# Optimization experiments

Measured on AMD Instinct MI355X. Metric: run time of the kernel, lower is better.

Reference implementation:

```python
import jax, jax.numpy as jnp
import numpy as np

EPS = 1e-5  # torch LayerNorm default
DT_RANK = 32  # ceil(d_model=512 / 16)


def layer_norm(x, g, b):
    mu = x.mean(-1, keepdims=True)
    var = x.var(-1, keepdims=True)
    return (x - mu) / jnp.sqrt(var + EPS) * g + b


def conv1d(x, w, b, pad):
    # x: (B, C, L), w: (O, I, K) -- torch Conv1d semantics
    y = jax.lax.conv_general_dilated(x, w, (1,), [(pad, pad)],
                                     dimension_numbers=('NCH', 'OIH', 'NCH'))
    return y + b[None, :, None]


def mamba(u, in_w, conv_w, conv_b, xproj_w, dt_w, dt_b, Alog, D, out_w, d_state, d_conv):
    # Faithful mamba_ssm Mamba block (no biases on in/x/out proj, RMS of official impl)
    Bsz, L, _ = u.shape
    xz = jnp.einsum('bld,ed->ble', u, in_w)          # (B, L, 2*Di)
    x, z = jnp.split(xz, 2, axis=-1)
    Di = x.shape[-1]
    # causal depthwise conv1d, truncated to L (padding=d_conv-1 on the left)
    xc = jax.lax.conv_general_dilated(x.transpose(0, 2, 1), conv_w[:, None, :], (1,),
                                      [(d_conv - 1, 0)],
                                      dimension_numbers=('NCH', 'OIH', 'NCH'),
                                      feature_group_count=Di)
    x = jax.nn.silu((xc + conv_b[None, :, None]).transpose(0, 2, 1))  # (B, L, Di)
    xdb = jnp.einsum('bld,ed->ble', x, xproj_w)       # (B, L, dt_rank + 2*N)
    dt = jax.nn.softplus(jnp.einsum('blr,dr->bld', xdb[..., :DT_RANK], dt_w) + dt_b)
    Bm = xdb[..., DT_RANK:DT_RANK + d_state]          # (B, L, N)
    Cm = xdb[..., DT_RANK + d_state:]                 # (B, L, N)
    A = -jnp.exp(Alog)                                # (Di, N)

    def step(h, ins):
        dt_t, x_t, B_t, C_t = ins                     # (B,Di),(B,Di),(B,N),(B,N)
        dA = jnp.exp(dt_t[..., None] * A)             # (B, Di, N)
        h = dA * h + (dt_t * x_t)[..., None] * B_t[:, None, :]
        y = (h * C_t[:, None, :]).sum(-1)             # (B, Di)
        return h, y

    h0 = jnp.zeros((Bsz, Di, d_state), u.dtype)
    xs = (dt.transpose(1, 0, 2), x.transpose(1, 0, 2),
          Bm.transpose(1, 0, 2), Cm.transpose(1, 0, 2))
    _, ys = jax.lax.scan(step, h0, xs)
    y = ys.transpose(1, 0, 2) + x * D                 # skip via D
    y = y * jax.nn.silu(z)
    return jnp.einsum('bld,od->blo', y, out_w)


def _forward(x, fe_w, fe_b, fe_ln_g, fe_ln_b, emb_ln_g, emb_ln_b,
             conv1_w, conv1_b, conv2_w, conv2_b,
             mf_in_w, mf_conv_w, mf_conv_b, mf_xproj_w, mf_dt_w, mf_dt_b, mf_Alog, mf_D, mf_out_w,
             mb_in_w, mb_conv_w, mb_conv_b, mb_xproj_w, mb_dt_w, mb_dt_b, mb_Alog, mb_D, mb_out_w,
             norm_g, norm_b, fc1_w, fc1_b, fc2_w, fc2_b):
    x = x.reshape(x.shape[0], 100, 23)
    # FrequencyEmbedding: rfft over a length-1 last dim == the signal itself; |.| then Linear+LN+ReLU
    id_mag = jnp.abs(x[..., :1])                      # (B, 100, 1)
    e = jax.nn.relu(layer_norm(id_mag @ fe_w.T + fe_b, fe_ln_g, fe_ln_b))
    id_embed = jax.nn.relu(layer_norm(e, emb_ln_g, emb_ln_b))  # outer LN+ReLU
    data = x[..., 1:].transpose(0, 2, 1)              # (B, 22, 100)
    f1 = jax.nn.relu(conv1d(data, conv1_w, conv1_b, 1))
    f2 = jax.nn.relu(conv1d(f1, conv2_w, conv2_b, 1)).transpose(0, 2, 1)  # (B,100,256)
    comb = jnp.concatenate([id_embed, f2], axis=-1)   # (B, 100, 512)
    fo = mamba(comb, mf_in_w, mf_conv_w, mf_conv_b, mf_xproj_w, mf_dt_w, mf_dt_b,
               mf_Alog, mf_D, mf_out_w, 16, 4)
    bo = mamba(comb[:, ::-1], mb_in_w, mb_conv_w, mb_conv_b, mb_xproj_w, mb_dt_w, mb_dt_b,
               mb_Alog, mb_D, mb_out_w, 8, 2)[:, ::-1]
    pooled = (fo + bo).max(axis=1)                    # (B, 512)
    pooled = layer_norm(pooled, norm_g, norm_b)       # self.norm (undefined in source; LN(512))
    h = jax.nn.relu(pooled @ fc1_w.T + fc1_b)
    return h @ fc2_w.T + fc2_b                        # (B, 4)


def setup_inputs() -> dict:
    key = jax.random.key(0)
    ks = iter(jax.random.split(key, 48))
    def n(shape, s=0.02):
        return jax.random.normal(next(ks), shape, jnp.float32) * s
    Di = 1024
    alog16 = jnp.log(jnp.tile(jnp.arange(1, 17, dtype=jnp.float32), (Di, 1)))
    alog8 = jnp.log(jnp.tile(jnp.arange(1, 9, dtype=jnp.float32), (Di, 1)))
    return {
        'x': jax.random.normal(next(ks), (512, 2300), jnp.float32),
        'fe_w': n((256, 1), 1.0), 'fe_b': jnp.zeros(256, jnp.float32),
        'fe_ln_g': jnp.ones(256, jnp.float32), 'fe_ln_b': jnp.zeros(256, jnp.float32),
        'emb_ln_g': jnp.ones(256, jnp.float32), 'emb_ln_b': jnp.zeros(256, jnp.float32),
        'conv1_w': n((128, 22, 3)), 'conv1_b': jnp.zeros(128, jnp.float32),
        'conv2_w': n((256, 128, 3)), 'conv2_b': jnp.zeros(256, jnp.float32),
        'mf_in_w': n((2 * Di, 512)), 'mf_conv_w': n((Di, 4)), 'mf_conv_b': jnp.zeros(Di, jnp.float32),
        'mf_xproj_w': n((32 + 2 * 16, Di)), 'mf_dt_w': n((Di, 32)), 'mf_dt_b': n((Di,), 0.1),
        'mf_Alog': alog16, 'mf_D': jnp.ones(Di, jnp.float32), 'mf_out_w': n((512, Di)),
        'mb_in_w': n((2 * Di, 512)), 'mb_conv_w': n((Di, 2)), 'mb_conv_b': jnp.zeros(Di, jnp.float32),
        'mb_xproj_w': n((32 + 2 * 8, Di)), 'mb_dt_w': n((Di, 32)), 'mb_dt_b': n((Di,), 0.1),
        'mb_Alog': alog8, 'mb_D': jnp.ones(Di, jnp.float32), 'mb_out_w': n((512, Di)),
        'norm_g': jnp.ones(512, jnp.float32), 'norm_b': jnp.zeros(512, jnp.float32),
        'fc1_w': n((128, 512)), 'fc1_b': jnp.zeros(128, jnp.float32),
        'fc2_w': n((4, 128)), 'fc2_b': jnp.zeros(4, jnp.float32),
    }


def reference(x, fe_w, fe_b, fe_ln_g, fe_ln_b, emb_ln_g, emb_ln_b,
              conv1_w, conv1_b, conv2_w, conv2_b,
              mf_in_w, mf_conv_w, mf_conv_b, mf_xproj_w, mf_dt_w, mf_dt_b, mf_Alog, mf_D, mf_out_w,
              mb_in_w, mb_conv_w, mb_conv_b, mb_xproj_w, mb_dt_w, mb_dt_b, mb_Alog, mb_D, mb_out_w,
              norm_g, norm_b, fc1_w, fc1_b, fc2_w, fc2_b):
    return _forward(x, fe_w, fe_b, fe_ln_g, fe_ln_b, emb_ln_g, emb_ln_b,
                    conv1_w, conv1_b, conv2_w, conv2_b,
                    mf_in_w, mf_conv_w, mf_conv_b, mf_xproj_w, mf_dt_w, mf_dt_b, mf_Alog, mf_D, mf_out_w,
                    mb_in_w, mb_conv_w, mb_conv_b, mb_xproj_w, mb_dt_w, mb_dt_b, mb_Alog, mb_D, mb_out_w,
                    norm_g, norm_b, fc1_w, fc1_b, fc2_w, fc2_b)
```

## Files before the change

kernel.cpp:

```cpp
#include <hip/hip_runtime.h>
#include <cstddef>
#include <cstdint>

#define BSZ 512
#define SEQ 100

typedef __bf16 bf16_t;
typedef __attribute__((ext_vector_type(8))) __bf16 bf16x8;
typedef __attribute__((ext_vector_type(4))) float f32x4;

__device__ __forceinline__ float sigmoidf_(float v){ return 1.f/(1.f + __expf(-v)); }
__device__ __forceinline__ float siluf_(float v){ return v * sigmoidf_(v); }
__device__ __forceinline__ float softplusf_(float v){ return (v > 20.f) ? v : __logf(1.f + __expf(v)); }

__global__ __launch_bounds__(256) void cvt_bf16_kernel(
    const float* __restrict__ src, bf16_t* __restrict__ dst, int n)
{
    int i = blockIdx.x*256 + threadIdx.x;
    if (i < n) dst[i] = (bf16_t)src[i];
}

__global__ __launch_bounds__(256) void prep_outw_kernel(
    const float* __restrict__ of, const float* __restrict__ ob, bf16_t* __restrict__ W)
{
    int i = blockIdx.x*256 + threadIdx.x;
    if (i < 512*2048){
        int o = i >> 11, k = i & 2047;
        W[i] = (bf16_t)((k < 1024) ? of[o*1024 + k] : ob[o*1024 + (k - 1024)]);
    }
}

__global__ __launch_bounds__(256) void prep_convw_kernel(
    const float* __restrict__ c1w, const float* __restrict__ c2w,
    bf16_t* __restrict__ W1p, bf16_t* __restrict__ W2p)
{
    int i = blockIdx.x*256 + threadIdx.x;
    if (i < 128*96){
        int o = i / 96, kk = i - o*96, k = kk >> 5, c = kk & 31;
        W1p[i] = (c < 22) ? (bf16_t)c1w[(o*22 + c)*3 + k] : (bf16_t)0.f;
    }
    if (i < 256*384){
        int o = i / 384, kk = i - o*384, k = kk >> 7, c = kk & 127;
        W2p[i] = (bf16_t)c2w[(o*128 + c)*3 + k];
    }
}

__global__ __launch_bounds__(256) void fe0_kernel(
    const float* __restrict__ x,
    const float* __restrict__ fe_w, const float* __restrict__ fe_b,
    const float* __restrict__ g1, const float* __restrict__ b1,
    const float* __restrict__ g2, const float* __restrict__ b2,
    bf16_t* __restrict__ comb, bf16_t* __restrict__ F0pad, bf16_t* __restrict__ F1pad)
{
    const int b = blockIdx.x;
    const int t = threadIdx.x;
    const int wv = t >> 6, lane = t & 63;

    float few[4], feb[4], lg1[4], lb1[4], lg2[4], lb2[4];
    #pragma unroll
    for (int q = 0; q < 4; ++q){
        int j = lane + 64*q;
        few[q] = fe_w[j]; feb[q] = fe_b[j];
        lg1[q] = g1[j];  lb1[q] = b1[j];
        lg2[q] = g2[j];  lb2[q] = b2[j];
    }
    for (int l = wv; l < SEQ; l += 4){
        float m = fabsf(x[(size_t)(b*SEQ + l)*23]);
        float e[4];
        float s1 = 0.f, s2 = 0.f;
        #pragma unroll
        for (int q = 0; q < 4; ++q){ e[q] = m*few[q] + feb[q]; s1 += e[q]; s2 += e[q]*e[q]; }
        #pragma unroll
        for (int off = 32; off > 0; off >>= 1){ s1 += __shfl_xor(s1, off); s2 += __shfl_xor(s2, off); }
        float mean = s1 * (1.f/256.f);
        float rstd = rsqrtf(s2*(1.f/256.f) - mean*mean + 1e-5f);
        s1 = 0.f; s2 = 0.f;
        #pragma unroll
        for (int q = 0; q < 4; ++q){
            e[q] = fmaxf((e[q]-mean)*rstd*lg1[q] + lb1[q], 0.f);
            s1 += e[q]; s2 += e[q]*e[q];
        }
        #pragma unroll
        for (int off = 32; off > 0; off >>= 1){ s1 += __shfl_xor(s1, off); s2 += __shfl_xor(s2, off); }
        mean = s1 * (1.f/256.f);
        rstd = rsqrtf(s2*(1.f/256.f) - mean*mean + 1e-5f);
        #pragma unroll
        for (int q = 0; q < 4; ++q){
            float v = fmaxf((e[q]-mean)*rstd*lg2[q] + lb2[q], 0.f);
            comb[(size_t)(b*SEQ + l)*512 + lane + 64*q] = (bf16_t)v;
        }
    }

    for (int idx = t; idx < 102*32; idx += 256){
        int r = idx >> 5, c = idx & 31;
        float v = 0.f;
        if (r >= 1 && r <= SEQ && c < 22) v = x[(size_t)(b*SEQ + r - 1)*23 + 1 + c];
        F0pad[(size_t)(b*102 + r)*32 + c] = (bf16_t)v;
    }
    if (t < 128) F1pad[(size_t)(b*102 + 0)*128 + t] = (bf16_t)0.f;
    else F1pad[(size_t)(b*102 + 101)*128 + (t - 128)] = (bf16_t)0.f;
}

__global__ __launch_bounds__(256) void gemm_conv_kernel(
    const bf16_t* __restrict__ Abase, int lda, int Az,
    const bf16_t* __restrict__ W, int K, int N,
    const float* __restrict__ bias,
    bf16_t* __restrict__ Cbase, int ldc, int Cb, int coff, int noff, int Mtot)
{
    __shared__ bf16_t As[128*32];
    __shared__ bf16_t Ws[128*32];
    const bf16_t* A = Abase + (size_t)blockIdx.z * Az;
    const int t = threadIdx.x;
    const int lane = t & 63, w = t >> 6;
    const int n0 = blockIdx.y * 128;
    const int rsub = lane >> 2, csub = lane & 3;
    const int col = lane & 15, quad = lane >> 4;
    const int wOffM = (w & 1) * 64, wOffN = (w >> 1) * 64;

    f32x4 acc[4][4];
    #pragma unroll
    for (int i = 0; i < 4; ++i)
        #pragma unroll
        for (int j = 0; j < 4; ++j)
            acc[i][j] = (f32x4){0.f, 0.f, 0.f, 0.f};

    for (int k0 = 0; k0 < K; k0 += 32){
        __syncthreads();
        #pragma unroll
        for (int q = 0; q < 2; ++q){
            const int rt = w*32 + q*16 + rsub;
            const int lq = csub ^ ((rt >> 1) & 3);
            int ra = (rt < Mtot) ? rt : (Mtot - 1);
            const bf16_t* ga = A + (size_t)ra*lda + k0 + lq*8;
            __builtin_amdgcn_global_load_lds(
                (const __attribute__((address_space(1))) void*)ga,
                (__attribute__((address_space(3))) void*)&As[(w*32 + q*16)*32], 16, 0, 0);
            const bf16_t* gw = W + (size_t)(n0 + rt)*K + k0 + lq*8;
            __builtin_amdgcn_global_load_lds(
                (const __attribute__((address_space(1))) void*)gw,
                (__attribute__((address_space(3))) void*)&Ws[(w*32 + q*16)*32], 16, 0, 0);
        }
        __syncthreads();

        bf16x8 af[4], bfv[4];
        #pragma unroll
        for (int i = 0; i < 4; ++i){
            const int ra = wOffM + i*16 + col;
            af[i]  = *(const bf16x8*)&As[ra*32 + (quad ^ ((ra >> 1) & 3))*8];
            const int rb = wOffN + i*16 + col;
            bfv[i] = *(const bf16x8*)&Ws[rb*32 + (quad ^ ((rb >> 1) & 3))*8];
        }
        #pragma unroll
        for (int i = 0; i < 4; ++i)
            #pragma unroll
            for (int j = 0; j < 4; ++j)
                acc[i][j] = __builtin_amdgcn_mfma_f32_16x16x32_bf16(af[i], bfv[j], acc[i][j], 0, 0, 0);
    }

    #pragma unroll
    for (int i = 0; i < 4; ++i){
        const int gmb = wOffM + i*16 + quad*4;
        #pragma unroll
        for (int j = 0; j < 4; ++j){
            const int gn = n0 + wOffN + j*16 + col;
            const float bb = bias[gn];
            #pragma unroll
            for (int r = 0; r < 4; ++r){
                const int gm = gmb + r;
                if (gm < Mtot){
                    float v = fmaxf(acc[i][j][r] + bb, 0.f);
                    Cbase[((size_t)blockIdx.z*Cb + coff + gm)*ldc + noff + gn] = (bf16_t)v;
                }
            }
        }
    }
}

__global__ __launch_bounds__(256) void gemm_in_kernel(
    const bf16_t* __restrict__ A, int lda, int Mtot,
    const bf16_t* __restrict__ W, int K,
    bf16_t* __restrict__ xy, bf16_t* __restrict__ z)
{
    __shared__ bf16_t As[128*32];
    __shared__ bf16_t Ws[128*32];
    const int t = threadIdx.x;
    const int lane = t & 63, w = t >> 6;
    const int m0 = blockIdx.x * 128, n0 = blockIdx.y * 128;
    const int rsub = lane >> 2, csub = lane & 3;
    const int col = lane & 15, quad = lane >> 4;
    const int wOffM = (w & 1) * 64, wOffN = (w >> 1) * 64;

    f32x4 acc[4][4];
    #pragma unroll
    for (int i = 0; i < 4; ++i)
        #pragma unroll
        for (int j = 0; j < 4; ++j)
            acc[i][j] = (f32x4){0.f, 0.f, 0.f, 0.f};

    for (int k0 = 0; k0 < K; k0 += 32){
        __syncthreads();
        #pragma unroll
        for (int q = 0; q < 2; ++q){
            const int rt = w*32 + q*16 + rsub;
            const int lq = csub ^ ((rt >> 1) & 3);
            int ra = m0 + rt; ra = (ra < Mtot) ? ra : (Mtot - 1);
            const bf16_t* ga = A + (size_t)ra*lda + k0 + lq*8;
            __builtin_amdgcn_global_load_lds(
                (const __attribute__((address_space(1))) void*)ga,
                (__attribute__((address_space(3))) void*)&As[(w*32 + q*16)*32], 16, 0, 0);
            const bf16_t* gw = W + (size_t)(n0 + rt)*K + k0 + lq*8;
            __builtin_amdgcn_global_load_lds(
                (const __attribute__((address_space(1))) void*)gw,
                (__attribute__((address_space(3))) void*)&Ws[(w*32 + q*16)*32], 16, 0, 0);
        }
        __syncthreads();

        bf16x8 af[4], bfv[4];
        #pragma unroll
        for (int i = 0; i < 4; ++i){
            const int ra = wOffM + i*16 + col;
            af[i]  = *(const bf16x8*)&As[ra*32 + (quad ^ ((ra >> 1) & 3))*8];
            const int rb = wOffN + i*16 + col;
            bfv[i] = *(const bf16x8*)&Ws[rb*32 + (quad ^ ((rb >> 1) & 3))*8];
        }
        #pragma unroll
        for (int i = 0; i < 4; ++i)
            #pragma unroll
            for (int j = 0; j < 4; ++j)
                acc[i][j] = __builtin_amdgcn_mfma_f32_16x16x32_bf16(af[i], bfv[j], acc[i][j], 0, 0, 0);
    }

    #pragma unroll
    for (int i = 0; i < 4; ++i){
        const int gmb = m0 + wOffM + i*16 + quad*4;
        #pragma unroll
        for (int j = 0; j < 4; ++j){
            const int gn = n0 + wOffN + j*16 + col;
            const int half = gn >> 11, within = gn & 2047;
            const size_t colx = (size_t)(half*1024 + (within & 1023));
            bf16_t* dst = (within < 1024) ? xy : z;
            #pragma unroll
            for (int r = 0; r < 4; ++r){
                const int gm = gmb + r;
                if (gm < Mtot)
                    dst[(size_t)gm*2048 + colx] = (bf16_t)acc[i][j][r];
            }
        }
    }
}

__global__ __launch_bounds__(256) void gemm_out_kernel(
    const bf16_t* __restrict__ A, int Mtot,
    const bf16_t* __restrict__ W,
    float* __restrict__ C)
{
    __shared__ bf16_t As[128*32];
    __shared__ bf16_t Ws[128*32];
    const int t = threadIdx.x;
    const int lane = t & 63, w = t >> 6;
    const int m0 = blockIdx.x * 128, n0 = blockIdx.y * 128;
    const int rsub = lane >> 2, csub = lane & 3;
    const int col = lane & 15, quad = lane >> 4;
    const int wOffM = (w & 1) * 64, wOffN = (w >> 1) * 64;
    const int K = 2048;

    f32x4 acc[4][4];
    #pragma unroll
    for (int i = 0; i < 4; ++i)
        #pragma unroll
        for (int j = 0; j < 4; ++j)
            acc[i][j] = (f32x4){0.f, 0.f, 0.f, 0.f};

    for (int k0 = 0; k0 < K; k0 += 32){
        __syncthreads();
        #pragma unroll
        for (int q = 0; q < 2; ++q){
            const int rt = w*32 + q*16 + rsub;
            const int lq = csub ^ ((rt >> 1) & 3);
            int ra = m0 + rt; ra = (ra < Mtot) ? ra : (Mtot - 1);
            const bf16_t* ga = A + (size_t)ra*K + k0 + lq*8;
            __builtin_amdgcn_global_load_lds(
                (const __attribute__((address_space(1))) void*)ga,
                (__attribute__((address_space(3))) void*)&As[(w*32 + q*16)*32], 16, 0, 0);
            const bf16_t* gw = W + (size_t)(n0 + rt)*K + k0 + lq*8;
            __builtin_amdgcn_global_load_lds(
                (const __attribute__((address_space(1))) void*)gw,
                (__attribute__((address_space(3))) void*)&Ws[(w*32 + q*16)*32], 16, 0, 0);
        }
        __syncthreads();

        bf16x8 af[4], bfv[4];
        #pragma unroll
        for (int i = 0; i < 4; ++i){
            const int ra = wOffM + i*16 + col;
            af[i]  = *(const bf16x8*)&As[ra*32 + (quad ^ ((ra >> 1) & 3))*8];
            const int rb = wOffN + i*16 + col;
            bfv[i] = *(const bf16x8*)&Ws[rb*32 + (quad ^ ((rb >> 1) & 3))*8];
        }
        #pragma unroll
        for (int i = 0; i < 4; ++i)
            #pragma unroll
            for (int j = 0; j < 4; ++j)
                acc[i][j] = __builtin_amdgcn_mfma_f32_16x16x32_bf16(af[i], bfv[j], acc[i][j], 0, 0, 0);
    }

    #pragma unroll
    for (int i = 0; i < 4; ++i){
        const int gmb = m0 + wOffM + i*16 + quad*4;
        #pragma unroll
        for (int j = 0; j < 4; ++j){
            const int gn = n0 + wOffN + j*16 + col;
            #pragma unroll
            for (int r = 0; r < 4; ++r){
                const int gm = gmb + r;
                if (gm < Mtot)
                    C[(size_t)gm*512 + gn] = acc[i][j][r];
            }
        }
    }
}

__global__ __launch_bounds__(256) void gemm_x_kernel(
    const bf16_t* __restrict__ xy,
    const bf16_t* __restrict__ Wf, const bf16_t* __restrict__ Wb,
    float* __restrict__ C)
{
    __shared__ bf16_t As[128*32];
    __shared__ bf16_t Ws[64*32];
    const int half = blockIdx.y;
    const bf16_t* A = xy + half*1024;
    const bf16_t* W = half ? Wb : Wf;
    const int N = half ? 48 : 64;
    const int t = threadIdx.x;
    const int lane = t & 63, w = t >> 6;
    const int m0 = blockIdx.x * 128;
    const int rsub = lane >> 2, csub = lane & 3;
    const int col = lane & 15, quad = lane >> 4;

    f32x4 acc[2][4];
    #pragma unroll
    for (int i = 0; i < 2; ++i)
        #pragma unroll
        for (int j = 0; j < 4; ++j)
            acc[i][j] = (f32x4){0.f, 0.f, 0.f, 0.f};

    for (int k0 = 0; k0 < 1024; k0 += 32){
        __syncthreads();
        #pragma unroll
        for (int q = 0; q < 2; ++q){
            const int rt = q*64 + w*16 + rsub;
            const int lq = csub ^ ((rt >> 1) & 3);
            const bf16_t* ga = A + (size_t)(m0 + rt)*2048 + k0 + lq*8;
            __builtin_amdgcn_global_load_lds(
                (const __attribute__((address_space(1))) void*)ga,
                (__attribute__((address_space(3))) void*)&As[(q*64 + w*16)*32], 16, 0, 0);
        }
        {
            const int rt = w*16 + rsub;
            const int lq = csub ^ ((rt >> 1) & 3);
            int rw = (rt < N) ? rt : (N - 1);
            const bf16_t* gw = W + (size_t)rw*1024 + k0 + lq*8;
            __builtin_amdgcn_global_load_lds(
                (const __attribute__((address_space(1))) void*)gw,
                (__attribute__((address_space(3))) void*)&Ws[(w*16)*32], 16, 0, 0);
        }
        __syncthreads();

        bf16x8 af[2], bfv[4];
        #pragma unroll
        for (int i = 0; i < 2; ++i){
            const int ra = w*32 + i*16 + col;
            af[i]  = *(const bf16x8*)&As[ra*32 + (quad ^ ((ra >> 1) & 3))*8];
        }
        #pragma unroll
        for (int j = 0; j < 4; ++j){
            const int rb = j*16 + col;
            bfv[j] = *(const bf16x8*)&Ws[rb*32 + (quad ^ ((rb >> 1) & 3))*8];
        }
        #pragma unroll
        for (int i = 0; i < 2; ++i)
            #pragma unroll
            for (int j = 0; j < 4; ++j)
                acc[i][j] = __builtin_amdgcn_mfma_f32_16x16x32_bf16(af[i], bfv[j], acc[i][j], 0, 0, 0);
    }

    #pragma unroll
    for (int i = 0; i < 2; ++i){
        const int gmb = m0 + w*32 + i*16 + quad*4;
        #pragma unroll
        for (int j = 0; j < 4; ++j){
            const int gn = j*16 + col;
            if (gn < N){
                #pragma unroll
                for (int r = 0; r < 4; ++r)
                    C[(size_t)(gmb + r)*128 + half*64 + gn] = acc[i][j][r];
            }
        }
    }
}

__global__ __launch_bounds__(256) void dt_kernel(
    const float* __restrict__ xdb,
    const float* __restrict__ dtwf, const float* __restrict__ dtbf,
    const float* __restrict__ dtwb, const float* __restrict__ dtbb,
    bf16_t* __restrict__ dtb)
{
    const int half = blockIdx.y >> 3;
    const int d = (blockIdx.y & 7)*128 + (threadIdx.x & 127);
    const int mslot = threadIdx.x >> 7;
    const int m0 = blockIdx.x * 16;
    __shared__ float sd[16*32];
    for (int i = threadIdx.x; i < 16*32; i += 256){
        int r = i >> 5, c = i & 31;
        sd[i] = xdb[(size_t)(m0 + r)*128 + half*64 + c];
    }
    const float* dw = half ? dtwb : dtwf;
    float w[32];
    #pragma unroll
    for (int r = 0; r < 32; ++r) w[r] = dw[d*32 + r];
    const float db = half ? dtbb[d] : dtbf[d];
    __syncthreads();
    #pragma unroll
    for (int i = 0; i < 8; ++i){
        const int row = mslot + i*2;
        const float* rp = &sd[row*32];
        float a = db;
        #pragma unroll
        for (int r = 0; r < 32; ++r) a += w[r]*rp[r];
        dtb[(size_t)(m0 + row)*2048 + half*1024 + d] = (bf16_t)softplusf_(a);
    }
}

template<int DC, bool REV>
__device__ __forceinline__ void conv_dev(bf16_t* base, const float* wsrc, float bias)
{
    float w[DC];
    #pragma unroll
    for (int k = 0; k < DC; ++k) w[k] = wsrc[k];
    float hist[DC-1];
    #pragma unroll
    for (int k = 0; k < DC-1; ++k) hist[k] = 0.f;
    const int step = REV ? -1 : 1;
    int l = REV ? (SEQ-1) : 0;
    for (int t0 = 0; t0 < SEQ; t0 += 10){
        float v[10];
        #pragma unroll
        for (int i = 0; i < 10; ++i) v[i] = (float)base[(size_t)(l + step*i)*2048];
        float o[10];
        #pragma unroll
        for (int i = 0; i < 10; ++i){
            float a = bias + w[DC-1]*v[i];
            #pragma unroll
            for (int j = 1; j < DC; ++j) a += w[DC-1-j]*hist[j-1];
            #pragma unroll
            for (int j = DC-2; j >= 1; --j) hist[j] = hist[j-1];
            hist[0] = v[i];
            o[i] = siluf_(a);
        }
        #pragma unroll
        for (int i = 0; i < 10; ++i)
            base[(size_t)(l + step*i)*2048] = (bf16_t)o[i];
        l += step*10;
    }
}

__global__ __launch_bounds__(256) void conv_silu_kernel(
    bf16_t* __restrict__ xy,
    const float* __restrict__ cwf, const float* __restrict__ cbf,
    const float* __restrict__ cwb, const float* __restrict__ cbb)
{
    const int gid = blockIdx.x*256 + threadIdx.x;
    const int b = gid >> 11, d2 = gid & 2047;
    const int half = d2 >> 10, d = d2 & 1023;
    bf16_t* base = xy + (size_t)b*SEQ*2048 + d2;
    if (half == 0) conv_dev<4, false>(base, cwf + d*4, cbf[d]);
    else           conv_dev<2, true >(base, cwb + d*2, cbb[d]);
}

template<int DS, bool REV>
__device__ __forceinline__ void scan_dev(
    bf16_t* __restrict__ xybase, const bf16_t* __restrict__ zbase,
    const bf16_t* __restrict__ tbase, const float* __restrict__ sx,
    const float* __restrict__ Arow, float Dd)
{
    float Av[DS], h[DS];
    #pragma unroll
    for (int s = 0; s < DS; ++s){ Av[s] = -__expf(Arow[s]); h[s] = 0.f; }
    bool structured = true;
    #pragma unroll
    for (int s = 1; s < DS; ++s)
        structured = structured && (fabsf(Av[s] - (float)(s+1)*Av[0]) <= 1e-4f*(float)(s+1));
    const float A0 = Av[0];
    const int step = REV ? -1 : 1;

    if (structured){
        int l = REV ? (SEQ-1) : 0;
        for (int t0 = 0; t0 < SEQ; t0 += 10){
            float xr[10], zr[10], tr[10];
            #pragma unroll
            for (int i = 0; i < 10; ++i){
                const size_t li = (size_t)(l + step*i);
                xr[i] = (float)xybase[li*2048];
                zr[i] = (float)zbase[li*2048];
                tr[i] = (float)tbase[li*2048];
            }
            #pragma unroll
            for (int i = 0; i < 10; ++i){
                const int li = l + step*i;
                const float4* sxl4 = (const float4*)&sx[li*2*DS];
                const float dtv = tr[i];
                const float dtx = dtv * xr[i];
                const float r = __expf(dtv*A0);
                float rp = r;
                float yv = 0.f;
                #pragma unroll
                for (int s4 = 0; s4 < DS/4; ++s4){
                    float4 Bv = sxl4[s4];
                    float4 Cv = sxl4[DS/4 + s4];
                    h[s4*4+0] = rp*h[s4*4+0] + dtx*Bv.x; yv += h[s4*4+0]*Cv.x; rp *= r;
                    h[s4*4+1] = rp*h[s4*4+1] + dtx*Bv.y; yv += h[s4*4+1]*Cv.y; rp *= r;
                    h[s4*4+2] = rp*h[s4*4+2] + dtx*Bv.z; yv += h[s4*4+2]*Cv.z; rp *= r;
                    h[s4*4+3] = rp*h[s4*4+3] + dtx*Bv.w; yv += h[s4*4+3]*Cv.w; rp *= r;
                }
                yv += xr[i]*Dd;
                yv *= siluf_(zr[i]);
                xybase[(size_t)li*2048] = (bf16_t)yv;
            }
            l += step*10;
        }
    } else {
        int l = REV ? (SEQ-1) : 0;
        for (int t0 = 0; t0 < SEQ; t0 += 10){
            float xr[10], zr[10], tr[10];
            #pragma unroll
            for (int i = 0; i < 10; ++i){
                const size_t li = (size_t)(l + step*i);
                xr[i] = (float)xybase[li*2048];
                zr[i] = (float)zbase[li*2048];
                tr[i] = (float)tbase[li*2048];
            }
            #pragma unroll
            for (int i = 0; i < 10; ++i){
                const int li = l + step*i;
                const float4* sxl4 = (const float4*)&sx[li*2*DS];
                const float dtv = tr[i];
                const float dtx = dtv * xr[i];
                float yv = 0.f;
                #pragma unroll
                for (int s4 = 0; s4 < DS/4; ++s4){
                    float4 Bv = sxl4[s4];
                    float4 Cv = sxl4[DS/4 + s4];
                    h[s4*4+0] = __expf(dtv*Av[s4*4+0])*h[s4*4+0] + dtx*Bv.x; yv += h[s4*4+0]*Cv.x;
                    h[s4*4+1] = __expf(dtv*Av[s4*4+1])*h[s4*4+1] + dtx*Bv.y; yv += h[s4*4+1]*Cv.y;
                    h[s4*4+2] = __expf(dtv*Av[s4*4+2])*h[s4*4+2] + dtx*Bv.z; yv += h[s4*4+2]*Cv.z;
                    h[s4*4+3] = __expf(dtv*Av[s4*4+3])*h[s4*4+3] + dtx*Bv.w; yv += h[s4*4+3]*Cv.w;
                }
                yv += xr[i]*Dd;
                yv *= siluf_(zr[i]);
                xybase[(size_t)li*2048] = (bf16_t)yv;
            }
            l += step*10;
        }
    }
}

__global__ __launch_bounds__(256) void scan_kernel(
    bf16_t* __restrict__ xy, const bf16_t* __restrict__ z,
    const bf16_t* __restrict__ dtb, const float* __restrict__ xdb,
    const float* __restrict__ Alogf, const float* __restrict__ Dpf,
    const float* __restrict__ Alogb, const float* __restrict__ Dpb)
{
    const int b = blockIdx.x >> 3, s8 = blockIdx.x & 7;
    __shared__ float sx[SEQ*32];
    const float4* src = (const float4*)(xdb + (size_t)b*SEQ*128);
    float4* dst = (float4*)sx;

    if (s8 < 4){
        for (int i = threadIdx.x; i < SEQ*8; i += 256){
            int row = i >> 3, c = i & 7;
            dst[row*8 + c] = src[row*32 + 8 + c];
        }
        const int d = (s8 << 8) + threadIdx.x;
        __syncthreads();
        scan_dev<16, false>(
            xy  + (size_t)b*SEQ*2048 + d,
            z   + (size_t)b*SEQ*2048 + d,
            dtb + (size_t)b*SEQ*2048 + d,
            sx, Alogf + d*16, Dpf[d]);
    } else {
        for (int i = threadIdx.x; i < SEQ*4; i += 256){
            int row = i >> 2, c = i & 3;
            dst[row*4 + c] = src[row*32 + 24 + c];
        }
        const int d = ((s8 - 4) << 8) + threadIdx.x;
        __syncthreads();
        scan_dev<8, true>(
            xy  + (size_t)b*SEQ*2048 + 1024 + d,
            z   + (size_t)b*SEQ*2048 + 1024 + d,
            dtb + (size_t)b*SEQ*2048 + 1024 + d,
            sx, Alogb + d*8, Dpb[d]);
    }
}

__global__ __launch_bounds__(256) void head_kernel(
    const float* __restrict__ acc,
    const float* __restrict__ ng, const float* __restrict__ nb,
    const float* __restrict__ w1, const float* __restrict__ b1,
    const float* __restrict__ w2, const float* __restrict__ b2,
    float* __restrict__ out)
{
    const int b = blockIdx.x, t = threadIdx.x;
    __shared__ float4 sm4[256];
    __shared__ float sp[512];
    __shared__ float sh2[256];
    __shared__ float sh[128];
    __shared__ float red1[4], red2[4];
    const float* base = acc + (size_t)b*SEQ*512;

    {
        const int c4 = t & 127, lh = t >> 7;
        float4 m = make_float4(-3.4e38f, -3.4e38f, -3.4e38f, -3.4e38f);
        for (int l = lh*50; l < lh*50 + 50; ++l){
            float4 v = ((const float4*)(base + (size_t)l*512))[c4];
            m.x = fmaxf(m.x, v.x); m.y = fmaxf(m.y, v.y);
            m.z = fmaxf(m.z, v.z); m.w = fmaxf(m.w, v.w);
        }
        sm4[t] = m;
    }
    __syncthreads();
    if (t < 128){
        float4 a = sm4[t], c = sm4[t + 128];
        ((float4*)sp)[t] = make_float4(fmaxf(a.x,c.x), fmaxf(a.y,c.y),
                                       fmaxf(a.z,c.z), fmaxf(a.w,c.w));
    }
    __syncthreads();

    float s1 = 0.f, s2 = 0.f;
    for (int o = t; o < 512; o += 256){ float v = sp[o]; s1 += v; s2 += v*v; }
    #pragma unroll
    for (int off = 32; off > 0; off >>= 1){ s1 += __shfl_xor(s1, off); s2 += __shfl_xor(s2, off); }
    const int wv = t >> 6, lane = t & 63;
    if (lane == 0){ red1[wv] = s1; red2[wv] = s2; }
    __syncthreads();
    if (t == 0){
        float a = 0.f, c = 0.f;
        for (int i = 0; i < 4; ++i){ a += red1[i]; c += red2[i]; }
        float mean = a * (1.f/512.f);
        float var = c * (1.f/512.f) - mean*mean;
        red1[0] = mean; red2[0] = rsqrtf(var + 1e-5f);
    }
    __syncthreads();
    const float mean = red1[0], rstd = red2[0];
    for (int o = t; o < 512; o += 256) sp[o] = (sp[o]-mean)*rstd*ng[o] + nb[o];
    __syncthreads();

    {
        const int o = t & 127, half = t >> 7;
        const float4* wrow = (const float4*)(w1 + (size_t)o*512 + half*256);
        const float4* sp4 = (const float4*)sp + half*64;
        float s = 0.f;
        #pragma unroll 8
        for (int j = 0; j < 64; ++j){
            float4 a = sp4[j], wq = wrow[j];
            s += a.x*wq.x + a.y*wq.y + a.z*wq.z + a.w*wq.w;
        }
        sh2[t] = s;
    }
    __syncthreads();
    if (t < 128) sh[t] = fmaxf(sh2[t] + sh2[t + 128] + b1[t], 0.f);
    __syncthreads();
    if (t < 4){
        float a = b2[t];
        for (int j = 0; j < 128; ++j) a += sh[j]*w2[t*128 + j];
        out[b*4 + t] = a;
    }
}

extern "C" void kernel_launch(void* const* d_in, const int* in_sizes, int n_in,
                              void* d_out, int out_size, void* d_ws, size_t ws_size,
                              hipStream_t stream)
{
    (void)in_sizes; (void)n_in; (void)out_size;
    const float* x        = (const float*)d_in[0];
    const float* fe_w     = (const float*)d_in[1];
    const float* fe_b     = (const float*)d_in[2];
    const float* fe_ln_g  = (const float*)d_in[3];
    const float* fe_ln_b  = (const float*)d_in[4];
    const float* emb_ln_g = (const float*)d_in[5];
    const float* emb_ln_b = (const float*)d_in[6];
    const float* conv1_w  = (const float*)d_in[7];
    const float* conv1_b  = (const float*)d_in[8];
    const float* conv2_w  = (const float*)d_in[9];
    const float* conv2_b  = (const float*)d_in[10];
    const float* mf_in_w  = (const float*)d_in[11];
    const float* mf_conv_w= (const float*)d_in[12];
    const float* mf_conv_b= (const float*)d_in[13];
    const float* mf_xproj = (const float*)d_in[14];
    const float* mf_dt_w  = (const float*)d_in[15];
    const float* mf_dt_b  = (const float*)d_in[16];
    const float* mf_Alog  = (const float*)d_in[17];
    const float* mf_D     = (const float*)d_in[18];
    const float* mf_out_w = (const float*)d_in[19];
    const float* mb_in_w  = (const float*)d_in[20];
    const float* mb_conv_w= (const float*)d_in[21];
    const float* mb_conv_b= (const float*)d_in[22];
    const float* mb_xproj = (const float*)d_in[23];
    const float* mb_dt_w  = (const float*)d_in[24];
    const float* mb_dt_b  = (const float*)d_in[25];
    const float* mb_Alog  = (const float*)d_in[26];
    const float* mb_D     = (const float*)d_in[27];
    const float* mb_out_w = (const float*)d_in[28];
    const float* norm_g   = (const float*)d_in[29];
    const float* norm_b   = (const float*)d_in[30];
    const float* fc1_w    = (const float*)d_in[31];
    const float* fc1_b    = (const float*)d_in[32];
    const float* fc2_w    = (const float*)d_in[33];
    const float* fc2_b    = (const float*)d_in[34];
    float* out = (float*)d_out;

    char* p = (char*)d_ws;
    bf16_t* w_in   = (bf16_t*)p; p += (size_t)4096*512*sizeof(bf16_t);
    bf16_t* w_out  = (bf16_t*)p; p += (size_t)512*2048*sizeof(bf16_t);
    bf16_t* w_xpf  = (bf16_t*)p; p += (size_t)64*1024*sizeof(bf16_t);
    bf16_t* w_xpb  = (bf16_t*)p; p += (size_t)48*1024*sizeof(bf16_t);
    bf16_t* W1p    = (bf16_t*)p; p += (size_t)128*96*sizeof(bf16_t);
    bf16_t* W2p    = (bf16_t*)p; p += (size_t)256*384*sizeof(bf16_t);
    bf16_t* comb_all = (bf16_t*)p; p += (size_t)BSZ*SEQ*512*sizeof(bf16_t);
    const size_t fixed_bytes = (size_t)(p - (char*)d_ws);

    const size_t per_b = (size_t)SEQ * (2048*2 + 2048*2 + 2048*2 + 128*4);
    const size_t budget = (ws_size > fixed_bytes) ? (ws_size - fixed_bytes) : 0;
    int Bc = BSZ;
    while (Bc > 64 && (size_t)Bc * per_b > budget) Bc >>= 1;
    const int nch = BSZ / Bc;
    const int M = Bc * SEQ;

    bf16_t* F0pad = (bf16_t*)p;
    bf16_t* F1pad = F0pad + (size_t)BSZ*102*32;
    bf16_t* xy   = (bf16_t*)p;               p += (size_t)M*2048*sizeof(bf16_t);
    bf16_t* z    = (bf16_t*)p;               p += (size_t)M*2048*sizeof(bf16_t);
    bf16_t* dtb  = (bf16_t*)p;               p += (size_t)M*2048*sizeof(bf16_t);
    float*  xdb  = (float*)p;
    float*  accb = (float*)dtb;

    cvt_bf16_kernel<<<(2048*512+255)/256, 256, 0, stream>>>(mf_in_w, w_in, 2048*512);
    cvt_bf16_kernel<<<(2048*512+255)/256, 256, 0, stream>>>(mb_in_w, w_in + (size_t)2048*512, 2048*512);
    prep_outw_kernel<<<(512*2048+255)/256, 256, 0, stream>>>(mf_out_w, mb_out_w, w_out);
    cvt_bf16_kernel<<<(64*1024+255)/256,  256, 0, stream>>>(mf_xproj, w_xpf, 64*1024);
    cvt_bf16_kernel<<<(48*1024+255)/256,  256, 0, stream>>>(mb_xproj, w_xpb, 48*1024);
    prep_convw_kernel<<<(256*384+255)/256, 256, 0, stream>>>(conv1_w, conv2_w, W1p, W2p);

    fe0_kernel<<<BSZ, 256, 0, stream>>>(x, fe_w, fe_b, fe_ln_g, fe_ln_b,
        emb_ln_g, emb_ln_b, comb_all, F0pad, F1pad);
    gemm_conv_kernel<<<dim3(1, 1, BSZ), 256, 0, stream>>>(
        F0pad, 32, 102*32, W1p, 96, 128, conv1_b, F1pad, 128, 102, 1, 0, SEQ);
    gemm_conv_kernel<<<dim3(1, 2, BSZ), 256, 0, stream>>>(
        F1pad, 128, 102*128, W2p, 384, 256, conv2_b, comb_all, 512, 100, 0, 256, SEQ);

    const int gm128 = M / 128;

    for (int c = 0; c < nch; ++c){
        const size_t b0 = (size_t)c * Bc;
        const bf16_t* comb = comb_all + b0*SEQ*512;

        gemm_in_kernel<<<dim3(gm128, 32), 256, 0, stream>>>(comb, 512, M, w_in, 512, xy, z);
        conv_silu_kernel<<<Bc*2048/256, 256, 0, stream>>>(xy, mf_conv_w, mf_conv_b,
                                                          mb_conv_w, mb_conv_b);
        gemm_x_kernel<<<dim3(gm128, 2), 256, 0, stream>>>(xy, w_xpf, w_xpb, xdb);
        dt_kernel<<<dim3(M/16, 16), 256, 0, stream>>>(xdb, mf_dt_w, mf_dt_b,
                                                      mb_dt_w, mb_dt_b, dtb);
        scan_kernel<<<Bc*8, 256, 0, stream>>>(xy, z, dtb, xdb,
                                              mf_Alog, mf_D, mb_Alog, mb_D);
        gemm_out_kernel<<<dim3(gm128, 4), 256, 0, stream>>>(xy, M, w_out, accb);
        head_kernel<<<Bc, 256, 0, stream>>>(accb, norm_g, norm_b, fc1_w, fc1_b,
                                            fc2_w, fc2_b, out + b0*4);
    }
}
```

Baseline: 1.598 ms.

## Split causal conv across sequence chunks and double-buffer scan input loads

The depthwise conv kernel now gives each thread a 25-step slice of the sequence instead of the full sequence. That creates four times more threads per channel, with halo values loaded up front and a block barrier placed before the in-place writes. The scan is restructured into groups of five timesteps with ping-pong register buffers, so the next group's x/z/dt loads are issued before the current group's compute. This is meant to raise parallelism and hide load latency, at the cost of more registers and a barrier that assumes the whole sequence for a batch lives in one block.

After: 1.708 ms. 6.9% more time.

```diff
diff --git a/kernel.cpp b/kernel.cpp
--- a/kernel.cpp
+++ b/kernel.cpp
@@ -431,88 +431,86 @@
     }
 }
 
-template<int DC, bool REV>
-__device__ __forceinline__ void conv_dev(bf16_t* base, const float* wsrc, float bias)
-{
-    float w[DC];
-    #pragma unroll
-    for (int k = 0; k < DC; ++k) w[k] = wsrc[k];
-    float hist[DC-1];
-    #pragma unroll
-    for (int k = 0; k < DC-1; ++k) hist[k] = 0.f;
-    const int step = REV ? -1 : 1;
-    int l = REV ? (SEQ-1) : 0;
-    for (int t0 = 0; t0 < SEQ; t0 += 10){
-        float v[10];
-        #pragma unroll
-        for (int i = 0; i < 10; ++i) v[i] = (float)base[(size_t)(l + step*i)*2048];
-        float o[10];
-        #pragma unroll
-        for (int i = 0; i < 10; ++i){
-            float a = bias + w[DC-1]*v[i];
-            #pragma unroll
-            for (int j = 1; j < DC; ++j) a += w[DC-1-j]*hist[j-1];
-            #pragma unroll
-            for (int j = DC-2; j >= 1; --j) hist[j] = hist[j-1];
-            hist[0] = v[i];
-            o[i] = siluf_(a);
-        }
-        #pragma unroll
-        for (int i = 0; i < 10; ++i)
-            base[(size_t)(l + step*i)*2048] = (bf16_t)o[i];
-        l += step*10;
-    }
-}
-
 __global__ __launch_bounds__(256) void conv_silu_kernel(
     bf16_t* __restrict__ xy,
     const float* __restrict__ cwf, const float* __restrict__ cbf,
     const float* __restrict__ cwb, const float* __restrict__ cbb)
 {
-    const int gid = blockIdx.x*256 + threadIdx.x;
-    const int b = gid >> 11, d2 = gid & 2047;
+    const int bb = blockIdx.x >> 5;
+    const int dblk = blockIdx.x & 31;
+    const int dl = threadIdx.x & 63, q = threadIdx.x >> 6;
+    const int d2 = dblk*64 + dl;
     const int half = d2 >> 10, d = d2 & 1023;
-    bf16_t* base = xy + (size_t)b*SEQ*2048 + d2;
-    if (half == 0) conv_dev<4, false>(base, cwf + d*4, cbf[d]);
-    else           conv_dev<2, true >(base, cwb + d*2, cbb[d]);
-}
-
-template<int DS, bool REV>
-__device__ __forceinline__ void scan_dev(
+    bf16_t* base = xy + (size_t)bb*SEQ*2048 + d2;
+    const int l0 = q*25;
+
+    if (half == 0){
+        const float w0 = cwf[d*4], w1 = cwf[d*4+1], w2 = cwf[d*4+2], w3 = cwf[d*4+3];
+        const float bia = cbf[d];
+        float v[28];
+        #pragma unroll
+        for (int i = 0; i < 28; ++i){
+            const int l = l0 - 3 + i;
+            v[i] = (l >= 0) ? (float)base[(size_t)l*2048] : 0.f;
+        }
+        __syncthreads();
+        #pragma unroll
+        for (int i = 0; i < 25; ++i){
+            float a = bia + w3*v[i+3] + w2*v[i+2] + w1*v[i+1] + w0*v[i];
+            base[(size_t)(l0+i)*2048] = (bf16_t)siluf_(a);
+        }
+    } else {
+        const float w0 = cwb[d*2], w1 = cwb[d*2+1];
+        const float bia = cbb[d];
+        float v[26];
+        #pragma unroll
+        for (int i = 0; i < 26; ++i){
+            const int l = l0 + i;
+            v[i] = (l < SEQ) ? (float)base[(size_t)l*2048] : 0.f;
+        }
+        __syncthreads();
+        #pragma unroll
+        for (int i = 0; i < 25; ++i){
+            float a = bia + w1*v[i] + w0*v[i+1];
+            base[(size_t)(l0+i)*2048] = (bf16_t)siluf_(a);
+        }
+    }
+}
+
+template<int DS, bool REV, bool STRUCT>
+__device__ __forceinline__ void scan_core(
     bf16_t* __restrict__ xybase, const bf16_t* __restrict__ zbase,
     const bf16_t* __restrict__ tbase, const float* __restrict__ sx,
-    const float* __restrict__ Arow, float Dd)
-{
-    float Av[DS], h[DS];
-    #pragma unroll
-    for (int s = 0; s < DS; ++s){ Av[s] = -__expf(Arow[s]); h[s] = 0.f; }
-    bool structured = true;
-    #pragma unroll
-    for (int s = 1; s < DS; ++s)
-        structured = structured && (fabsf(Av[s] - (float)(s+1)*Av[0]) <= 1e-4f*(float)(s+1));
+    const float* __restrict__ Av, float Dd)
+{
+    float h[DS];
+    #pragma unroll
+    for (int s = 0; s < DS; ++s) h[s] = 0.f;
+    const int step = REV ? -1 : 1;
+    const int l0 = REV ? (SEQ-1) : 0;
     const float A0 = Av[0];
-    const int step = REV ? -1 : 1;
-
-    if (structured){
-        int l = REV ? (SEQ-1) : 0;
-        for (int t0 = 0; t0 < SEQ; t0 += 10){
-            float xr[10], zr[10], tr[10];
-            #pragma unroll
-            for (int i = 0; i < 10; ++i){
-                const size_t li = (size_t)(l + step*i);
-                xr[i] = (float)xybase[li*2048];
-                zr[i] = (float)zbase[li*2048];
-                tr[i] = (float)tbase[li*2048];
-            }
-            #pragma unroll
-            for (int i = 0; i < 10; ++i){
-                const int li = l + step*i;
-                const float4* sxl4 = (const float4*)&sx[li*2*DS];
-                const float dtv = tr[i];
-                const float dtx = dtv * xr[i];
+    constexpr int G = 5;
+
+    auto loadg = [&](int lbase, float* xr, float* zr, float* tr){
+        #pragma unroll
+        for (int i = 0; i < G; ++i){
+            const size_t li = (size_t)(lbase + step*i);
+            xr[i] = (float)xybase[li*2048];
+            zr[i] = (float)zbase[li*2048];
+            tr[i] = (float)tbase[li*2048];
+        }
+    };
+    auto computeg = [&](int lbase, const float* xr, const float* zr, const float* tr){
+        #pragma unroll
+        for (int i = 0; i < G; ++i){
+            const int li = lbase + step*i;
+            const float4* sxl4 = (const float4*)&sx[li*2*DS];
+            const float dtv = tr[i];
+            const float dtx = dtv * xr[i];
+            float yv = 0.f;
+            if (STRUCT){
                 const float r = __expf(dtv*A0);
                 float rp = r;
-                float yv = 0.f;
                 #pragma unroll
                 for (int s4 = 0; s4 < DS/4; ++s4){
                     float4 Bv = sxl4[s4];
@@ -522,30 +520,7 @@
                     h[s4*4+2] = rp*h[s4*4+2] + dtx*Bv.z; yv += h[s4*4+2]*Cv.z; rp *= r;
                     h[s4*4+3] = rp*h[s4*4+3] + dtx*Bv.w; yv += h[s4*4+3]*Cv.w; rp *= r;
                 }
-                yv += xr[i]*Dd;
-                yv *= siluf_(zr[i]);
-                xybase[(size_t)li*2048] = (bf16_t)yv;
-            }
-            l += step*10;
-        }
-    } else {
-        int l = REV ? (SEQ-1) : 0;
-        for (int t0 = 0; t0 < SEQ; t0 += 10){
-            float xr[10], zr[10], tr[10];
-            #pragma unroll
-            for (int i = 0; i < 10; ++i){
-                const size_t li = (size_t)(l + step*i);
-                xr[i] = (float)xybase[li*2048];
-                zr[i] = (float)zbase[li*2048];
-                tr[i] = (float)tbase[li*2048];
-            }
-            #pragma unroll
-            for (int i = 0; i < 10; ++i){
-                const int li = l + step*i;
-                const float4* sxl4 = (const float4*)&sx[li*2*DS];
-                const float dtv = tr[i];
-                const float dtx = dtv * xr[i];
-                float yv = 0.f;
+            } else {
                 #pragma unroll
                 for (int s4 = 0; s4 < DS/4; ++s4){
                     float4 Bv = sxl4[s4];
@@ -555,13 +530,41 @@
                     h[s4*4+2] = __expf(dtv*Av[s4*4+2])*h[s4*4+2] + dtx*Bv.z; yv += h[s4*4+2]*Cv.z;
                     h[s4*4+3] = __expf(dtv*Av[s4*4+3])*h[s4*4+3] + dtx*Bv.w; yv += h[s4*4+3]*Cv.w;
                 }
-                yv += xr[i]*Dd;
-                yv *= siluf_(zr[i]);
-                xybase[(size_t)li*2048] = (bf16_t)yv;
             }
-            l += step*10;
-        }
-    }
+            yv += xr[i]*Dd;
+            yv *= siluf_(zr[i]);
+            xybase[(size_t)li*2048] = (bf16_t)yv;
+        }
+    };
+
+    float xa[G], za[G], ta[G], xb[G], zb[G], tb[G];
+    loadg(l0, xa, za, ta);
+    for (int gp = 0; gp < SEQ/(2*G); ++gp){
+        const int le = l0 + step*(2*gp)*G;
+        const int lo = le + step*G;
+        loadg(lo, xb, zb, tb);
+        computeg(le, xa, za, ta);
+        if (gp + 1 < SEQ/(2*G))
+            loadg(lo + step*G, xa, za, ta);
+        computeg(lo, xb, zb, tb);
+    }
+}
+
+template<int DS, bool REV>
+__device__ __forceinline__ void scan_dev(
+    bf16_t* __restrict__ xybase, const bf16_t* __restrict__ zbase,
+    const bf16_t* __restrict__ tbase, const float* __restrict__ sx,
+    const float* __restrict__ Arow, float Dd)
+{
+    float Av[DS];
+    #pragma unroll
+    for (int s = 0; s < DS; ++s) Av[s] = -__expf(Arow[s]);
+    bool structured = true;
+    #pragma unroll
+    for (int s = 1; s < DS; ++s)
+        structured = structured && (fabsf(Av[s] - (float)(s+1)*Av[0]) <= 1e-4f*(float)(s+1));
+    if (structured) scan_core<DS, REV, true >(xybase, zbase, tbase, sx, Av, Dd);
+    else            scan_core<DS, REV, false>(xybase, zbase, tbase, sx, Av, Dd);
 }
 
 __global__ __launch_bounds__(256) void scan_kernel(
@@ -764,8 +767,8 @@
         const bf16_t* comb = comb_all + b0*SEQ*512;
 
         gemm_in_kernel<<<dim3(gm128, 32), 256, 0, stream>>>(comb, 512, M, w_in, 512, xy, z);
-        conv_silu_kernel<<<Bc*2048/256, 256, 0, stream>>>(xy, mf_conv_w, mf_conv_b,
-                                                          mb_conv_w, mb_conv_b);
+        conv_silu_kernel<<<Bc*32, 256, 0, stream>>>(xy, mf_conv_w, mf_conv_b,
+                                                    mb_conv_w, mb_conv_b);
         gemm_x_kernel<<<dim3(gm128, 2), 256, 0, stream>>>(xy, w_xpf, w_xpb, xdb);
         dt_kernel<<<dim3(M/16, 16), 256, 0, stream>>>(xdb, mf_dt_w, mf_dt_b,
                                                       mb_dt_w, mb_dt_b, dtb);
```

## Stage scan inputs through LDS stripes with vectorized coalesced loads

Applied to the files above, without the earlier changes.

The selective-scan kernel now loads x, z and dt for 25 timesteps at a time into shared memory using float4 loads across the block, runs the recurrence from LDS, and writes the outputs back with float4 stores. Before, each thread did scalar 2-byte strided global loads per timestep. The goal is wider memory transactions and more memory parallelism. In exchange it adds block-wide syncs per stripe, takes more shared memory (which may lower occupancy), and loses overlap between loading and computing.

After: 1.669 ms. 1.04x slower.

```diff
diff --git a/kernel.cpp b/kernel.cpp
--- a/kernel.cpp
+++ b/kernel.cpp
@@ -477,89 +477,93 @@
     else           conv_dev<2, true >(base, cwb + d*2, cbb[d]);
 }
 
+#define STRIPE 25
+
+template<int DS, bool REV, bool STRUCT>
+__device__ __forceinline__ void scan_stripe_compute(
+    bf16_t* __restrict__ SX, const bf16_t* __restrict__ SZ,
+    const bf16_t* __restrict__ ST, const float* __restrict__ sxBC,
+    int ls, int t, const float* __restrict__ Av, float A0, float Dd,
+    float* __restrict__ h)
+{
+    #pragma unroll
+    for (int ii = 0; ii < STRIPE; ++ii){
+        const int i = REV ? (STRIPE-1-ii) : ii;
+        const int l = ls + i;
+        const float xv = (float)SX[i*256 + t];
+        const float zv = (float)SZ[i*256 + t];
+        const float dtv = (float)ST[i*256 + t];
+        const float4* sxl4 = (const float4*)&sxBC[l*2*DS];
+        const float dtx = dtv * xv;
+        float yv = 0.f;
+        if (STRUCT){
+            const float r = __expf(dtv*A0);
+            float rp = r;
+            #pragma unroll
+            for (int s4 = 0; s4 < DS/4; ++s4){
+                float4 Bv = sxl4[s4];
+                float4 Cv = sxl4[DS/4 + s4];
+                h[s4*4+0] = rp*h[s4*4+0] + dtx*Bv.x; yv += h[s4*4+0]*Cv.x; rp *= r;
+                h[s4*4+1] = rp*h[s4*4+1] + dtx*Bv.y; yv += h[s4*4+1]*Cv.y; rp *= r;
+                h[s4*4+2] = rp*h[s4*4+2] + dtx*Bv.z; yv += h[s4*4+2]*Cv.z; rp *= r;
+                h[s4*4+3] = rp*h[s4*4+3] + dtx*Bv.w; yv += h[s4*4+3]*Cv.w; rp *= r;
+            }
+        } else {
+            #pragma unroll
+            for (int s4 = 0; s4 < DS/4; ++s4){
+                float4 Bv = sxl4[s4];
+                float4 Cv = sxl4[DS/4 + s4];
+                h[s4*4+0] = __expf(dtv*Av[s4*4+0])*h[s4*4+0] + dtx*Bv.x; yv += h[s4*4+0]*Cv.x;
+                h[s4*4+1] = __expf(dtv*Av[s4*4+1])*h[s4*4+1] + dtx*Bv.y; yv += h[s4*4+1]*Cv.y;
+                h[s4*4+2] = __expf(dtv*Av[s4*4+2])*h[s4*4+2] + dtx*Bv.z; yv += h[s4*4+2]*Cv.z;
+                h[s4*4+3] = __expf(dtv*Av[s4*4+3])*h[s4*4+3] + dtx*Bv.w; yv += h[s4*4+3]*Cv.w;
+            }
+        }
+        yv += xv*Dd;
+        yv *= siluf_(zv);
+        SX[i*256 + t] = (bf16_t)yv;
+    }
+}
+
 template<int DS, bool REV>
-__device__ __forceinline__ void scan_dev(
-    bf16_t* __restrict__ xybase, const bf16_t* __restrict__ zbase,
-    const bf16_t* __restrict__ tbase, const float* __restrict__ sx,
-    const float* __restrict__ Arow, float Dd)
-{
-    float Av[DS], h[DS];
-    #pragma unroll
-    for (int s = 0; s < DS; ++s){ Av[s] = -__expf(Arow[s]); h[s] = 0.f; }
+__device__ __forceinline__ void scan_striped(
+    bf16_t* __restrict__ xyg, const bf16_t* __restrict__ zg,
+    const bf16_t* __restrict__ dtg,
+    bf16_t* __restrict__ SX, bf16_t* __restrict__ SZ, bf16_t* __restrict__ ST,
+    const float* __restrict__ sxBC,
+    int t, const float* __restrict__ Arow, float Dd)
+{
+    float Av[DS];
+    #pragma unroll
+    for (int s = 0; s < DS; ++s) Av[s] = -__expf(Arow[s]);
     bool structured = true;
     #pragma unroll
     for (int s = 1; s < DS; ++s)
         structured = structured && (fabsf(Av[s] - (float)(s+1)*Av[0]) <= 1e-4f*(float)(s+1));
     const float A0 = Av[0];
-    const int step = REV ? -1 : 1;
-
-    if (structured){
-        int l = REV ? (SEQ-1) : 0;
-        for (int t0 = 0; t0 < SEQ; t0 += 10){
-            float xr[10], zr[10], tr[10];
-            #pragma unroll
-            for (int i = 0; i < 10; ++i){
-                const size_t li = (size_t)(l + step*i);
-                xr[i] = (float)xybase[li*2048];
-                zr[i] = (float)zbase[li*2048];
-                tr[i] = (float)tbase[li*2048];
-            }
-            #pragma unroll
-            for (int i = 0; i < 10; ++i){
-                const int li = l + step*i;
-                const float4* sxl4 = (const float4*)&sx[li*2*DS];
-                const float dtv = tr[i];
-                const float dtx = dtv * xr[i];
-                const float r = __expf(dtv*A0);
-                float rp = r;
-                float yv = 0.f;
-                #pragma unroll
-                for (int s4 = 0; s4 < DS/4; ++s4){
-                    float4 Bv = sxl4[s4];
-                    float4 Cv = sxl4[DS/4 + s4];
-                    h[s4*4+0] = rp*h[s4*4+0] + dtx*Bv.x; yv += h[s4*4+0]*Cv.x; rp *= r;
-                    h[s4*4+1] = rp*h[s4*4+1] + dtx*Bv.y; yv += h[s4*4+1]*Cv.y; rp *= r;
-                    h[s4*4+2] = rp*h[s4*4+2] + dtx*Bv.z; yv += h[s4*4+2]*Cv.z; rp *= r;
-                    h[s4*4+3] = rp*h[s4*4+3] + dtx*Bv.w; yv += h[s4*4+3]*Cv.w; rp *= r;
-                }
-                yv += xr[i]*Dd;
-                yv *= siluf_(zr[i]);
-                xybase[(size_t)li*2048] = (bf16_t)yv;
-            }
-            l += step*10;
-        }
-    } else {
-        int l = REV ? (SEQ-1) : 0;
-        for (int t0 = 0; t0 < SEQ; t0 += 10){
-            float xr[10], zr[10], tr[10];
-            #pragma unroll
-            for (int i = 0; i < 10; ++i){
-                const size_t li = (size_t)(l + step*i);
-                xr[i] = (float)xybase[li*2048];
-                zr[i] = (float)zbase[li*2048];
-                tr[i] = (float)tbase[li*2048];
-            }
-            #pragma unroll
-            for (int i = 0; i < 10; ++i){
-                const int li = l + step*i;
-                const float4* sxl4 = (const float4*)&sx[li*2*DS];
-                const float dtv = tr[i];
-                const float dtx = dtv * xr[i];
-                float yv = 0.f;
-                #pragma unroll
-                for (int s4 = 0; s4 < DS/4; ++s4){
-                    float4 Bv = sxl4[s4];
-                    float4 Cv = sxl4[DS/4 + s4];
-                    h[s4*4+0] = __expf(dtv*Av[s4*4+0])*h[s4*4+0] + dtx*Bv.x; yv += h[s4*4+0]*Cv.x;
-                    h[s4*4+1] = __expf(dtv*Av[s4*4+1])*h[s4*4+1] + dtx*Bv.y; yv += h[s4*4+1]*Cv.y;
-                    h[s4*4+2] = __expf(dtv*Av[s4*4+2])*h[s4*4+2] + dtx*Bv.z; yv += h[s4*4+2]*Cv.z;
-                    h[s4*4+3] = __expf(dtv*Av[s4*4+3])*h[s4*4+3] + dtx*Bv.w; yv += h[s4*4+3]*Cv.w;
-                }
-                yv += xr[i]*Dd;
-                yv *= siluf_(zr[i]);
-                xybase[(size_t)li*2048] = (bf16_t)yv;
-            }
-            l += step*10;
+    float h[DS];
+    #pragma unroll
+    for (int s = 0; s < DS; ++s) h[s] = 0.f;
+
+    for (int sidx = 0; sidx < SEQ/STRIPE; ++sidx){
+        const int s = REV ? (SEQ/STRIPE - 1 - sidx) : sidx;
+        const int ls = s * STRIPE;
+        __syncthreads();
+        for (int i = t; i < STRIPE*32; i += 256){
+            const int row = i >> 5, f4 = i & 31;
+            ((float4*)SX)[i] = *((const float4*)(xyg + (size_t)(ls + row)*2048) + f4);
+            ((float4*)SZ)[i] = *((const float4*)(zg  + (size_t)(ls + row)*2048) + f4);
+            ((float4*)ST)[i] = *((const float4*)(dtg + (size_t)(ls + row)*2048) + f4);
+        }
+        __syncthreads();
+        if (structured)
+            scan_stripe_compute<DS, REV, true >(SX, SZ, ST, sxBC, ls, t, Av, A0, Dd, h);
+        else
+            scan_stripe_compute<DS, REV, false>(SX, SZ, ST, sxBC, ls, t, Av, A0, Dd, h);
+        __syncthreads();
+        for (int i = t; i < STRIPE*32; i += 256){
+            const int row = i >> 5, f4 = i & 31;
+            *((float4*)(xyg + (size_t)(ls + row)*2048) + f4) = ((const float4*)SX)[i];
         }
     }
 }
@@ -571,34 +575,32 @@
     const float* __restrict__ Alogb, const float* __restrict__ Dpb)
 {
     const int b = blockIdx.x >> 3, s8 = blockIdx.x & 7;
-    __shared__ float sx[SEQ*32];
+    const int t = threadIdx.x;
+    __shared__ float sxBC[SEQ*32];
+    __shared__ bf16_t SX[STRIPE*256];
+    __shared__ bf16_t SZ[STRIPE*256];
+    __shared__ bf16_t ST[STRIPE*256];
     const float4* src = (const float4*)(xdb + (size_t)b*SEQ*128);
-    float4* dst = (float4*)sx;
+    float4* dst = (float4*)sxBC;
 
     if (s8 < 4){
-        for (int i = threadIdx.x; i < SEQ*8; i += 256){
+        for (int i = t; i < SEQ*8; i += 256){
             int row = i >> 3, c = i & 7;
             dst[row*8 + c] = src[row*32 + 8 + c];
         }
-        const int d = (s8 << 8) + threadIdx.x;
-        __syncthreads();
-        scan_dev<16, false>(
-            xy  + (size_t)b*SEQ*2048 + d,
-            z   + (size_t)b*SEQ*2048 + d,
-            dtb + (size_t)b*SEQ*2048 + d,
-            sx, Alogf + d*16, Dpf[d]);
+        const int d = (s8 << 8) + t;
+        const size_t off = (size_t)b*SEQ*2048 + (size_t)s8*256;
+        scan_striped<16, false>(xy + off, z + off, dtb + off,
+                                SX, SZ, ST, sxBC, t, Alogf + d*16, Dpf[d]);
     } else {
-        for (int i = threadIdx.x; i < SEQ*4; i += 256){
+        for (int i = t; i < SEQ*4; i += 256){
             int row = i >> 2, c = i & 3;
             dst[row*4 + c] = src[row*32 + 24 + c];
         }
-        const int d = ((s8 - 4) << 8) + threadIdx.x;
-        __syncthreads();
-        scan_dev<8, true>(
-            xy  + (size_t)b*SEQ*2048 + 1024 + d,
-            z   + (size_t)b*SEQ*2048 + 1024 + d,
-            dtb + (size_t)b*SEQ*2048 + 1024 + d,
-            sx, Alogb + d*8, Dpb[d]);
+        const int d = ((s8 - 4) << 8) + t;
+        const size_t off = (size_t)b*SEQ*2048 + 1024 + (size_t)(s8 - 4)*256;
+        scan_striped<8, true>(xy + off, z + off, dtb + off,
+                              SX, SZ, ST, sxBC, t, Alogb + d*8, Dpb[d]);
     }
 }
 
```
